# Optimization experiments

Measured on AMD Instinct MI355X. Metric: run time of the kernel, lower is better.

## Reference

```python
import jax, jax.numpy as jnp
import numpy as np

B, S, H = 8, 2048, 1024
W_SCALE = 0.02  # small init keeps the 2048-step recurrence numerically stable


def setup_inputs() -> dict:
    key = jax.random.key(0)
    ks = jax.random.split(key, 6)
    x = jax.random.normal(ks[0], (B, S, H), dtype=jnp.float32)
    h0 = jnp.zeros((B, H), dtype=jnp.float32)
    # torch Linear y = x @ W.T + b; we store pre-transposed [in, out] matrices
    W_in = jax.random.normal(ks[1], (H, 3 * H), dtype=jnp.float32) * W_SCALE
    b_in = jnp.zeros((3 * H,), dtype=jnp.float32)
    W_gate = jax.random.normal(ks[2], (H, 2 * H), dtype=jnp.float32) * W_SCALE
    b_gate = jnp.zeros((2 * H,), dtype=jnp.float32)
    W_rec = jax.random.normal(ks[3], (H, H), dtype=jnp.float32) * W_SCALE
    b_rec = jnp.zeros((H,), dtype=jnp.float32)
    W_out = jax.random.normal(ks[4], (H, H), dtype=jnp.float32) * W_SCALE
    b_out = jnp.zeros((H,), dtype=jnp.float32)
    return {"x": x, "h0": h0, "W_in": W_in, "b_in": b_in,
            "W_gate": W_gate, "b_gate": b_gate, "W_rec": W_rec, "b_rec": b_rec,
            "W_out": W_out, "b_out": b_out}


def reference(x, h0, W_in, b_in, W_gate, b_gate, W_rec, b_rec, W_out, b_out):
    # input projection, chunk into u, v, w and activate (swish)
    feats = x @ W_in + b_in                      # [B,S,3H]
    u, v, w = jnp.split(feats, 3, axis=-1)
    drive = jax.nn.silu(u) * jax.nn.silu(v) + w  # (1-gate) branch, [B,S,H]

    def step(h, d_t):
        g = h @ W_gate + b_gate                  # [B,2H]
        gv, gt = jnp.split(g, 2, axis=-1)
        gate = jax.nn.sigmoid(gv) * jax.nn.silu(gt)  # GLU gate
        new_h = gate * (h @ W_rec + b_rec) + (1.0 - gate) * d_t
        # dropout is identity in eval mode
        return new_h, new_h

    final_h, hs = jax.lax.scan(step, h0, jnp.swapaxes(drive, 0, 1))  # hs: [S,B,H]
    hs = jnp.swapaxes(hs, 0, 1)                  # [B,S,H]
    out = hs @ W_out + b_out                     # per-timestep output_proj, batched
    return out, final_h
```

## Files before the change

### kernel.cpp

```cpp
#include <hip/hip_runtime.h>

typedef short short8 __attribute__((ext_vector_type(8)));
typedef __bf16 bf16x8 __attribute__((ext_vector_type(8)));
typedef float f32x4 __attribute__((ext_vector_type(4)));
typedef float f32x4v __attribute__((ext_vector_type(4)));
typedef unsigned short u16x4 __attribute__((ext_vector_type(4)));
typedef unsigned int uint2v __attribute__((ext_vector_type(2)));
typedef unsigned long long u64;

__device__ __forceinline__ unsigned short f2b(float f) {
  unsigned x = __builtin_bit_cast(unsigned, f);
  x = x + 0x7fffu + ((x >> 16) & 1u);
  return (unsigned short)(x >> 16);
}
__device__ __forceinline__ float b2f(unsigned short u) {
  unsigned x = ((unsigned)u) << 16;
  return __builtin_bit_cast(float, x);
}
__device__ __forceinline__ f32x4 mfma16(short8 a, short8 b, f32x4 c) {
  return __builtin_amdgcn_mfma_f32_16x16x32_bf16(
      __builtin_bit_cast(bf16x8, a), __builtin_bit_cast(bf16x8, b), c, 0, 0, 0);
}
typedef const __attribute__((address_space(1))) void* gas_p;
typedef __attribute__((address_space(3))) void* las_p;
__device__ __forceinline__ void gload_lds16(const void* g, void* l) {
  __builtin_amdgcn_global_load_lds((gas_p)g, (las_p)l, 16, 0, 0);
}

__global__ __launch_bounds__(256) void k_cvt_bf16(const float* __restrict__ in,
                                                  unsigned short* __restrict__ out,
                                                  int n4) {
  int i = blockIdx.x * 256 + threadIdx.x;
  if (i >= n4) return;
  f32x4v v = *(const f32x4v*)(in + (size_t)i * 4);
  u16x4 o;
  o[0] = f2b(v[0]); o[1] = f2b(v[1]); o[2] = f2b(v[2]); o[3] = f2b(v[3]);
  *(u16x4*)(out + (size_t)i * 4) = o;
}

__global__ __launch_bounds__(256) void k_init_hq(const float* __restrict__ h0,
                                                 unsigned int* __restrict__ hq) {
  int idx = blockIdx.x * 256 + threadIdx.x;
  if (idx >= 8192) return;
  int b = idx >> 10, i = idx & 1023;
  hq[(size_t)b * 2048 + i] = (unsigned int)f2b(h0[idx]);
  hq[(size_t)b * 2048 + 1024 + i] = 0u;
}

__global__ __launch_bounds__(256) void k_transpose_bf16(const float* __restrict__ in,
                                                        unsigned short* __restrict__ out,
                                                        int R, int C) {
  __shared__ unsigned short tile[32][33];
  int c0 = blockIdx.x * 32, r0 = blockIdx.y * 32;
  int tx = threadIdx.x & 31, ty = threadIdx.x >> 5;
#pragma unroll
  for (int i = 0; i < 4; i++) {
    int r = ty + i * 8;
    tile[r][tx] = f2b(in[(size_t)(r0 + r) * C + c0 + tx]);
  }
  __syncthreads();
#pragma unroll
  for (int i = 0; i < 4; i++) {
    int rr = ty + i * 8;
    out[(size_t)(c0 + rr) * R + r0 + tx] = tile[tx][rr];
  }
}

__global__ __launch_bounds__(256) void k_gemm_drive(const unsigned short* __restrict__ xb,
                                                    const unsigned short* __restrict__ WinT,
                                                    const float* __restrict__ b_in,
                                                    unsigned short* __restrict__ drive) {
  __shared__ unsigned short At[128 * 32];
  __shared__ unsigned short Bt[3][64 * 32];
  const int tid = threadIdx.x;
  const int w = tid >> 6, l = tid & 63;
  const int wm = w >> 1, wn = w & 1;
  const int lr = l & 15, lk = (l >> 4) * 8;
  const int m0 = blockIdx.x * 128;
  const int j0 = blockIdx.y * 64;
  f32x4 acc[3][4][2];
#pragma unroll
  for (int s = 0; s < 3; s++)
#pragma unroll
    for (int mi = 0; mi < 4; mi++)
#pragma unroll
      for (int ni = 0; ni < 2; ni++)
#pragma unroll
        for (int e = 0; e < 4; e++) acc[s][mi][ni][e] = 0.f;

  const int sr = tid >> 2;
  const int skb = (tid & 3) * 8;
  for (int kt = 0; kt < 32; kt++) {
    const int k0 = kt * 32;
    gload_lds16(xb + (size_t)(m0 + sr) * 1024 + k0 + skb, &At[w * 512]);
    gload_lds16(xb + (size_t)(m0 + 64 + sr) * 1024 + k0 + skb, &At[2048 + w * 512]);
#pragma unroll
    for (int s = 0; s < 3; s++)
      gload_lds16(WinT + (size_t)(s * 1024 + j0 + sr) * 1024 + k0 + skb, &Bt[s][w * 512]);
    __syncthreads();
    short8 Af[4], Bf[3][2];
#pragma unroll
    for (int mi = 0; mi < 4; mi++)
      Af[mi] = *(const short8*)&At[(wm * 64 + mi * 16 + lr) * 32 + lk];
#pragma unroll
    for (int s = 0; s < 3; s++)
#pragma unroll
      for (int ni = 0; ni < 2; ni++)
        Bf[s][ni] = *(const short8*)&Bt[s][(wn * 32 + ni * 16 + lr) * 32 + lk];
#pragma unroll
    for (int s = 0; s < 3; s++)
#pragma unroll
      for (int mi = 0; mi < 4; mi++)
#pragma unroll
        for (int ni = 0; ni < 2; ni++)
          acc[s][mi][ni] = mfma16(Af[mi], Bf[s][ni], acc[s][mi][ni]);
    __syncthreads();
  }
#pragma unroll
  for (int ni = 0; ni < 2; ni++) {
    const int c = j0 + wn * 32 + ni * 16 + lr;
    const float bu = b_in[c], bv = b_in[1024 + c], bw = b_in[2048 + c];
#pragma unroll
    for (int mi = 0; mi < 4; mi++) {
      const int r0 = m0 + wm * 64 + mi * 16 + (l >> 4) * 4;
#pragma unroll
      for (int e = 0; e < 4; e++) {
        float u = acc[0][mi][ni][e] + bu;
        float v = acc[1][mi][ni][e] + bv;
        float wv = acc[2][mi][ni][e] + bw;
        float su = u / (1.f + __expf(-u));
        float sv = v / (1.f + __expf(-v));
        drive[(size_t)(r0 + e) * 1024 + c] = f2b(su * sv + wv);
      }
    }
  }
}

__global__ __launch_bounds__(1024, 4) void k_scan(const unsigned short* __restrict__ WgT,
                                                  const unsigned short* __restrict__ WrT,
                                                  const float* __restrict__ b_gate,
                                                  const float* __restrict__ b_rec,
                                                  const unsigned short* __restrict__ drive,
                                                  unsigned int* __restrict__ hq,
                                                  unsigned short* __restrict__ hs,
                                                  float* __restrict__ final_h) {
  const int g = blockIdx.x;
  const int r = g >> 5;
  const int s = g & 31;
  const int tid = threadIdx.x;
  const int w = tid >> 6, l = tid & 63;

  __shared__ unsigned int tileh[2][512];
  __shared__ float buf[2][4][3][32];

  const int mat = w >> 2, kq = w & 3;
  const int lr = l & 15, ko = l >> 4;
  const bool av = (lr == 0);
  short8 Breg[2][8];
  if (w < 12) {
    const unsigned short* WT = (mat == 2) ? WrT : WgT;
    const int rowbase = ((mat == 1) ? 1024 : 0) + s * 32;
#pragma unroll
    for (int tile = 0; tile < 2; ++tile)
#pragma unroll
      for (int ks = 0; ks < 8; ++ks)
        Breg[tile][ks] = *(const short8*)&WT[(size_t)(rowbase + tile * 16 + lr) * 1024 +
                                             kq * 256 + ks * 32 + ko * 8];
  }

  const bool isld = tid >= 768;
  const int q = tid - 768;

  const bool isfin = tid < 32;
  const int fcol = s * 32 + tid;
  float bgv = 0.f, bgt = 0.f, brc = 0.f;
  if (isfin) { bgv = b_gate[fcol]; bgt = b_gate[1024 + fcol]; brc = b_rec[fcol]; }

  for (int t = 0; t < 2048; ++t) {
    const int p = t & 1;
    unsigned short dpf[2] = {0, 0};
    if (isfin) {
      dpf[0] = drive[(size_t)((2 * r) * 2048 + t) * 1024 + fcol];
      dpf[1] = drive[(size_t)((2 * r + 1) * 2048 + t) * 1024 + fcol];
    }

#pragma unroll
    for (int ab = 0; ab < 2; ++ab) {
      const int b = 2 * r + ab;

      if (isld) {
        const unsigned tg = (unsigned)t;
        const u64* hb = (const u64*)(hq + (size_t)(b * 2 + p) * 1024);
        u64 v0 = 0, v1 = 0;
        unsigned pend = 3u;
        do {
          if (pend & 1u)
            v0 = __hip_atomic_load(hb + 2 * q, __ATOMIC_RELAXED,
                                   __HIP_MEMORY_SCOPE_AGENT);
          if (pend & 2u)
            v1 = __hip_atomic_load(hb + 2 * q + 1, __ATOMIC_RELAXED,
                                   __HIP_MEMORY_SCOPE_AGENT);
          unsigned np = 0;
          if ((((unsigned)v0 >> 16) != tg) | (((unsigned)(v0 >> 32) >> 16) != tg))
            np |= 1u;
          if ((((unsigned)v1 >> 16) != tg) | (((unsigned)(v1 >> 32) >> 16) != tg))
            np |= 2u;
          pend = np;
        } while (pend);
        uint2v pk;
        pk[0] = __builtin_amdgcn_perm((unsigned)(v0 >> 32), (unsigned)v0, 0x05040100u);
        pk[1] = __builtin_amdgcn_perm((unsigned)(v1 >> 32), (unsigned)v1, 0x05040100u);
        *(uint2v*)&tileh[ab][2 * q] = pk;
      }
      __syncthreads();

      if (w < 12) {
        f32x4 a0, a1;
#pragma unroll
        for (int e = 0; e < 4; ++e) { a0[e] = 0.f; a1[e] = 0.f; }
        const char* base = (const char*)&tileh[ab][0] + kq * 512 + ko * 16;
#pragma unroll
        for (int ks = 0; ks < 8; ++ks) {
          short8 Af;
#pragma unroll
          for (int e = 0; e < 8; ++e) Af[e] = 0;
          if (av) Af = *(const short8*)(base + ks * 64);
          a0 = mfma16(Af, Breg[0][ks], a0);
          a1 = mfma16(Af, Breg[1][ks], a1);
        }
        if (l < 16) {
          buf[ab][kq][mat][l] = a0[0];
          buf[ab][kq][mat][16 + l] = a1[0];
        }
      }
      __syncthreads();

      if (isfin) {
        const float gv = ((buf[ab][0][0][tid] + buf[ab][1][0][tid]) +
                          (buf[ab][2][0][tid] + buf[ab][3][0][tid])) + bgv;
        const float gt = ((buf[ab][0][1][tid] + buf[ab][1][1][tid]) +
                          (buf[ab][2][1][tid] + buf[ab][3][1][tid])) + bgt;
        const float rc = ((buf[ab][0][2][tid] + buf[ab][1][2][tid]) +
                          (buf[ab][2][2][tid] + buf[ab][3][2][tid])) + brc;
        const float sgv = 1.f / (1.f + __expf(-gv));
        const float sgt = 1.f / (1.f + __expf(-gt));
        const float gate = sgv * gt * sgt;
        const float nh = gate * rc + (1.f - gate) * b2f(dpf[ab]);
        const unsigned short nhb = f2b(nh);
        __hip_atomic_store(hq + (size_t)(b * 2 + (p ^ 1)) * 1024 + fcol,
                           (((unsigned)(t + 1)) << 16) | (unsigned)nhb,
                           __ATOMIC_RELAXED, __HIP_MEMORY_SCOPE_AGENT);
        hs[(size_t)(b * 2048 + t) * 1024 + fcol] = nhb;
        if (t == 2047) final_h[b * 1024 + fcol] = nh;
      }
    }
  }
}

__global__ __launch_bounds__(256) void k_gemm_out(const unsigned short* __restrict__ hs,
                                                  const unsigned short* __restrict__ WoT,
                                                  const float* __restrict__ b_out,
                                                  float* __restrict__ out) {
  __shared__ unsigned short At[128 * 32];
  __shared__ unsigned short Bt[128 * 32];
  const int tid = threadIdx.x;
  const int w = tid >> 6, l = tid & 63;
  const int wm = w >> 1, wn = w & 1;
  const int lr = l & 15, lk = (l >> 4) * 8;
  const int m0 = blockIdx.x * 128;
  const int n0 = blockIdx.y * 128;
  f32x4 acc[4][4];
#pragma unroll
  for (int mi = 0; mi < 4; mi++)
#pragma unroll
    for (int ni = 0; ni < 4; ni++)
#pragma unroll
      for (int e = 0; e < 4; e++) acc[mi][ni][e] = 0.f;

  const int sr = tid >> 2;
  const int skb = (tid & 3) * 8;
  for (int kt = 0; kt < 32; kt++) {
    const int k0 = kt * 32;
    gload_lds16(hs + (size_t)(m0 + sr) * 1024 + k0 + skb, &At[w * 512]);
    gload_lds16(hs + (size_t)(m0 + 64 + sr) * 1024 + k0 + skb, &At[2048 + w * 512]);
    gload_lds16(WoT + (size_t)(n0 + sr) * 1024 + k0 + skb, &Bt[w * 512]);
    gload_lds16(WoT + (size_t)(n0 + 64 + sr) * 1024 + k0 + skb, &Bt[2048 + w * 512]);
    __syncthreads();
    short8 Af[4], Bf[4];
#pragma unroll
    for (int mi = 0; mi < 4; mi++)
      Af[mi] = *(const short8*)&At[(wm * 64 + mi * 16 + lr) * 32 + lk];
#pragma unroll
    for (int ni = 0; ni < 4; ni++)
      Bf[ni] = *(const short8*)&Bt[(wn * 64 + ni * 16 + lr) * 32 + lk];
#pragma unroll
    for (int mi = 0; mi < 4; mi++)
#pragma unroll
      for (int ni = 0; ni < 4; ni++)
        acc[mi][ni] = mfma16(Af[mi], Bf[ni], acc[mi][ni]);
    __syncthreads();
  }
#pragma unroll
  for (int ni = 0; ni < 4; ni++) {
    const int c = n0 + wn * 64 + ni * 16 + lr;
    const float bo = b_out[c];
#pragma unroll
    for (int mi = 0; mi < 4; mi++) {
      const int r0 = m0 + wm * 64 + mi * 16 + (l >> 4) * 4;
#pragma unroll
      for (int e = 0; e < 4; e++)
        out[(size_t)(r0 + e) * 1024 + c] = acc[mi][ni][e] + bo;
    }
  }
}

extern "C" void kernel_launch(void* const* d_in, const int* in_sizes, int n_in,
                              void* d_out, int out_size, void* d_ws, size_t ws_size,
                              hipStream_t stream) {
  const float* x      = (const float*)d_in[0];
  const float* h0     = (const float*)d_in[1];
  const float* W_in   = (const float*)d_in[2];
  const float* b_in   = (const float*)d_in[3];
  const float* W_gate = (const float*)d_in[4];
  const float* b_gate = (const float*)d_in[5];
  const float* W_rec  = (const float*)d_in[6];
  const float* b_rec  = (const float*)d_in[7];
  const float* W_out  = (const float*)d_in[8];
  const float* b_out  = (const float*)d_in[9];
  float* outp = (float*)d_out;

  size_t off = 0;
  auto alloc = [&](size_t bytes) {
    void* p = (char*)d_ws + off;
    off += (bytes + 255) & ~(size_t)255;
    return p;
  };
  unsigned short* xb    = (unsigned short*)alloc((size_t)16777216 * 2);
  unsigned short* WinT  = (unsigned short*)alloc((size_t)3072 * 1024 * 2);
  unsigned short* WgT   = (unsigned short*)alloc((size_t)2048 * 1024 * 2);
  unsigned short* WrT   = (unsigned short*)alloc((size_t)1024 * 1024 * 2);
  unsigned short* WoT   = (unsigned short*)alloc((size_t)1024 * 1024 * 2);
  unsigned short* drive = (unsigned short*)alloc((size_t)16777216 * 2);
  unsigned short* hs    = (unsigned short*)alloc((size_t)16777216 * 2);
  unsigned int*   hq    = (unsigned int*)alloc((size_t)8 * 2 * 1024 * 4);

  k_cvt_bf16<<<16384, 256, 0, stream>>>(x, xb, 4194304);
  k_transpose_bf16<<<dim3(96, 32), 256, 0, stream>>>(W_in, WinT, 1024, 3072);
  k_transpose_bf16<<<dim3(64, 32), 256, 0, stream>>>(W_gate, WgT, 1024, 2048);
  k_transpose_bf16<<<dim3(32, 32), 256, 0, stream>>>(W_rec, WrT, 1024, 1024);
  k_transpose_bf16<<<dim3(32, 32), 256, 0, stream>>>(W_out, WoT, 1024, 1024);
  k_init_hq<<<32, 256, 0, stream>>>(h0, hq);

  k_gemm_drive<<<dim3(128, 16), 256, 0, stream>>>(xb, WinT, b_in, drive);
  k_scan<<<128, 1024, 0, stream>>>(WgT, WrT, b_gate, b_rec, drive, hq,
                                   hs, outp + 16777216);
  k_gemm_out<<<dim3(128, 8), 256, 0, stream>>>(hs, WoT, b_out, outp);
}
```

Measured before the change: 5.029 ms.

## Interleave two batch rows in scan to overlap polling with MFMA

Restructures the persistent recurrence kernel to 512 threads with 6 MFMA waves, each holding a half-K slice of weights, and 2 polling waves that each fetch 4 packed h values. Polling for one batch row's next hidden state is now placed in the same phase as the finish of the other row, so cross-block latency is hidden behind the other row's work. Drive values are also staged into shared memory by the idle polling waves. This trades more registers per wave and a different sync pattern for less serialized wait per timestep.

```diff
diff --git a/kernel.cpp b/kernel.cpp
--- a/kernel.cpp
+++ b/kernel.cpp
@@ -5,7 +5,7 @@
 typedef float f32x4 __attribute__((ext_vector_type(4)));
 typedef float f32x4v __attribute__((ext_vector_type(4)));
 typedef unsigned short u16x4 __attribute__((ext_vector_type(4)));
-typedef unsigned int uint2v __attribute__((ext_vector_type(2)));
+typedef unsigned int u32x4 __attribute__((ext_vector_type(4)));
 typedef unsigned long long u64;
 
 __device__ __forceinline__ unsigned short f2b(float f) {
@@ -136,124 +136,141 @@
   }
 }
 
-__global__ __launch_bounds__(1024, 4) void k_scan(const unsigned short* __restrict__ WgT,
-                                                  const unsigned short* __restrict__ WrT,
-                                                  const float* __restrict__ b_gate,
-                                                  const float* __restrict__ b_rec,
-                                                  const unsigned short* __restrict__ drive,
-                                                  unsigned int* __restrict__ hq,
-                                                  unsigned short* __restrict__ hs,
-                                                  float* __restrict__ final_h) {
+__global__ __launch_bounds__(512, 1) void k_scan(const unsigned short* __restrict__ WgT,
+                                                 const unsigned short* __restrict__ WrT,
+                                                 const float* __restrict__ b_gate,
+                                                 const float* __restrict__ b_rec,
+                                                 const unsigned short* __restrict__ drive,
+                                                 unsigned int* __restrict__ hq,
+                                                 unsigned short* __restrict__ hs,
+                                                 float* __restrict__ final_h) {
   const int g = blockIdx.x;
   const int r = g >> 5;
   const int s = g & 31;
   const int tid = threadIdx.x;
   const int w = tid >> 6, l = tid & 63;
+  const int bA = 2 * r, bB = 2 * r + 1;
 
   __shared__ unsigned int tileh[2][512];
-  __shared__ float buf[2][4][3][32];
-
-  const int mat = w >> 2, kq = w & 3;
+  __shared__ float buf[2][2][3][32];
+  __shared__ unsigned short dd[2][32];
+
+  const int mat = w >> 1, kh = w & 1;
   const int lr = l & 15, ko = l >> 4;
   const bool av = (lr == 0);
-  short8 Breg[2][8];
-  if (w < 12) {
+  short8 Breg0[16], Breg1[16];
+  if (w < 6) {
     const unsigned short* WT = (mat == 2) ? WrT : WgT;
     const int rowbase = ((mat == 1) ? 1024 : 0) + s * 32;
 #pragma unroll
-    for (int tile = 0; tile < 2; ++tile)
-#pragma unroll
-      for (int ks = 0; ks < 8; ++ks)
-        Breg[tile][ks] = *(const short8*)&WT[(size_t)(rowbase + tile * 16 + lr) * 1024 +
-                                             kq * 256 + ks * 32 + ko * 8];
-  }
-
-  const bool isld = tid >= 768;
-  const int q = tid - 768;
-
-  const bool isfin = tid < 32;
-  const int fcol = s * 32 + tid;
+    for (int ks = 0; ks < 16; ++ks) {
+      Breg0[ks] = *(const short8*)&WT[(size_t)(rowbase + lr) * 1024 +
+                                      kh * 512 + ks * 32 + ko * 8];
+      Breg1[ks] = *(const short8*)&WT[(size_t)(rowbase + 16 + lr) * 1024 +
+                                      kh * 512 + ks * 32 + ko * 8];
+    }
+  }
+
+  const bool ispl = (w >= 6);
+  const int P = ((w - 6) << 6) | l;
+
+  const bool isfin = (w == 0) && (l < 32);
+  const int fcol = s * 32 + l;
   float bgv = 0.f, bgt = 0.f, brc = 0.f;
   if (isfin) { bgv = b_gate[fcol]; bgt = b_gate[1024 + fcol]; brc = b_rec[fcol]; }
 
+  auto poll4 = [&](const u64* base, unsigned tg, unsigned int* dst) {
+    const u64* p = base + 4 * P;
+    u64 v[4];
+    unsigned pend = 0xFu;
+    do {
+      unsigned np = 0;
+#pragma unroll
+      for (int j = 0; j < 4; ++j)
+        if ((pend >> j) & 1)
+          v[j] = __hip_atomic_load(p + j, __ATOMIC_RELAXED,
+                                   __HIP_MEMORY_SCOPE_AGENT);
+#pragma unroll
+      for (int j = 0; j < 4; ++j)
+        if ((pend >> j) & 1) {
+          if ((((unsigned)v[j] >> 16) != tg) |
+              (((unsigned)(v[j] >> 32) >> 16) != tg))
+            np |= 1u << j;
+        }
+      pend = np;
+    } while (pend);
+    u32x4 pk;
+#pragma unroll
+    for (int j = 0; j < 4; ++j)
+      pk[j] = __builtin_amdgcn_perm((unsigned)(v[j] >> 32), (unsigned)v[j],
+                                    0x05040100u);
+    *(u32x4*)&dst[4 * P] = pk;
+  };
+
+  auto mfma_phase = [&](int X) {
+    f32x4 a0, a1, c0, c1;
+#pragma unroll
+    for (int e = 0; e < 4; ++e) { a0[e] = 0.f; a1[e] = 0.f; c0[e] = 0.f; c1[e] = 0.f; }
+    const char* base = (const char*)&tileh[X][0] + kh * 1024 + ko * 16;
+#pragma unroll
+    for (int ks = 0; ks < 16; ++ks) {
+      short8 Af;
+#pragma unroll
+      for (int e = 0; e < 8; ++e) Af[e] = 0;
+      if (av) Af = *(const short8*)(base + ks * 64);
+      if (ks & 1) { a1 = mfma16(Af, Breg0[ks], a1); c1 = mfma16(Af, Breg1[ks], c1); }
+      else        { a0 = mfma16(Af, Breg0[ks], a0); c0 = mfma16(Af, Breg1[ks], c0); }
+    }
+    if (l < 16) {
+      buf[X][kh][mat][l] = a0[0] + a1[0];
+      buf[X][kh][mat][16 + l] = c0[0] + c1[0];
+    }
+  };
+
+  auto finish = [&](int X, int b, int t) {
+    const float gv = buf[X][0][0][l] + buf[X][1][0][l] + bgv;
+    const float gt = buf[X][0][1][l] + buf[X][1][1][l] + bgt;
+    const float rc = buf[X][0][2][l] + buf[X][1][2][l] + brc;
+    const float sgv = 1.f / (1.f + __expf(-gv));
+    const float sgt = 1.f / (1.f + __expf(-gt));
+    const float gate = sgv * gt * sgt;
+    const float nh = gate * rc + (1.f - gate) * b2f(dd[X][l]);
+    const unsigned short nhb = f2b(nh);
+    __hip_atomic_store(hq + (size_t)(b * 2 + ((t + 1) & 1)) * 1024 + fcol,
+                       (((unsigned)(t + 1)) << 16) | (unsigned)nhb,
+                       __ATOMIC_RELAXED, __HIP_MEMORY_SCOPE_AGENT);
+    hs[(size_t)(b * 2048 + t) * 1024 + fcol] = nhb;
+    if (t == 2047) final_h[b * 1024 + fcol] = nh;
+  };
+
+  if (ispl) {
+    poll4((const u64*)(hq + (size_t)(bA * 2) * 1024), 0u, &tileh[0][0]);
+    poll4((const u64*)(hq + (size_t)(bB * 2) * 1024), 0u, &tileh[1][0]);
+  }
+  __syncthreads();
+
   for (int t = 0; t < 2048; ++t) {
-    const int p = t & 1;
-    unsigned short dpf[2] = {0, 0};
-    if (isfin) {
-      dpf[0] = drive[(size_t)((2 * r) * 2048 + t) * 1024 + fcol];
-      dpf[1] = drive[(size_t)((2 * r + 1) * 2048 + t) * 1024 + fcol];
-    }
-
-#pragma unroll
-    for (int ab = 0; ab < 2; ++ab) {
-      const int b = 2 * r + ab;
-
-      if (isld) {
-        const unsigned tg = (unsigned)t;
-        const u64* hb = (const u64*)(hq + (size_t)(b * 2 + p) * 1024);
-        u64 v0 = 0, v1 = 0;
-        unsigned pend = 3u;
-        do {
-          if (pend & 1u)
-            v0 = __hip_atomic_load(hb + 2 * q, __ATOMIC_RELAXED,
-                                   __HIP_MEMORY_SCOPE_AGENT);
-          if (pend & 2u)
-            v1 = __hip_atomic_load(hb + 2 * q + 1, __ATOMIC_RELAXED,
-                                   __HIP_MEMORY_SCOPE_AGENT);
-          unsigned np = 0;
-          if ((((unsigned)v0 >> 16) != tg) | (((unsigned)(v0 >> 32) >> 16) != tg))
-            np |= 1u;
-          if ((((unsigned)v1 >> 16) != tg) | (((unsigned)(v1 >> 32) >> 16) != tg))
-            np |= 2u;
-          pend = np;
-        } while (pend);
-        uint2v pk;
-        pk[0] = __builtin_amdgcn_perm((unsigned)(v0 >> 32), (unsigned)v0, 0x05040100u);
-        pk[1] = __builtin_amdgcn_perm((unsigned)(v1 >> 32), (unsigned)v1, 0x05040100u);
-        *(uint2v*)&tileh[ab][2 * q] = pk;
-      }
-      __syncthreads();
-
-      if (w < 12) {
-        f32x4 a0, a1;
-#pragma unroll
-        for (int e = 0; e < 4; ++e) { a0[e] = 0.f; a1[e] = 0.f; }
-        const char* base = (const char*)&tileh[ab][0] + kq * 512 + ko * 16;
-#pragma unroll
-        for (int ks = 0; ks < 8; ++ks) {
-          short8 Af;
-#pragma unroll
-          for (int e = 0; e < 8; ++e) Af[e] = 0;
-          if (av) Af = *(const short8*)(base + ks * 64);
-          a0 = mfma16(Af, Breg[0][ks], a0);
-          a1 = mfma16(Af, Breg[1][ks], a1);
-        }
-        if (l < 16) {
-          buf[ab][kq][mat][l] = a0[0];
-          buf[ab][kq][mat][16 + l] = a1[0];
-        }
-      }
-      __syncthreads();
-
-      if (isfin) {
-        const float gv = ((buf[ab][0][0][tid] + buf[ab][1][0][tid]) +
-                          (buf[ab][2][0][tid] + buf[ab][3][0][tid])) + bgv;
-        const float gt = ((buf[ab][0][1][tid] + buf[ab][1][1][tid]) +
-                          (buf[ab][2][1][tid] + buf[ab][3][1][tid])) + bgt;
-        const float rc = ((buf[ab][0][2][tid] + buf[ab][1][2][tid]) +
-                          (buf[ab][2][2][tid] + buf[ab][3][2][tid])) + brc;
-        const float sgv = 1.f / (1.f + __expf(-gv));
-        const float sgt = 1.f / (1.f + __expf(-gt));
-        const float gate = sgv * gt * sgt;
-        const float nh = gate * rc + (1.f - gate) * b2f(dpf[ab]);
-        const unsigned short nhb = f2b(nh);
-        __hip_atomic_store(hq + (size_t)(b * 2 + (p ^ 1)) * 1024 + fcol,
-                           (((unsigned)(t + 1)) << 16) | (unsigned)nhb,
-                           __ATOMIC_RELAXED, __HIP_MEMORY_SCOPE_AGENT);
-        hs[(size_t)(b * 2048 + t) * 1024 + fcol] = nhb;
-        if (t == 2047) final_h[b * 1024 + fcol] = nh;
-      }
-    }
+    if (w < 6) mfma_phase(0);
+    else if (l < 32) {
+      if (w == 6) dd[0][l] = drive[((size_t)bA * 2048 + t) * 1024 + s * 32 + l];
+      else        dd[1][l] = drive[((size_t)bB * 2048 + t) * 1024 + s * 32 + l];
+    }
+    __syncthreads();
+
+    if (isfin) finish(0, bA, t);
+    if (ispl && t > 0)
+      poll4((const u64*)(hq + (size_t)(bB * 2 + (t & 1)) * 1024), (unsigned)t,
+            &tileh[1][0]);
+    __syncthreads();
+
+    if (w < 6) mfma_phase(1);
+    __syncthreads();
+
+    if (isfin) finish(1, bB, t);
+    if (ispl && t < 2047)
+      poll4((const u64*)(hq + (size_t)(bA * 2 + ((t + 1) & 1)) * 1024),
+            (unsigned)(t + 1), &tileh[0][0]);
+    __syncthreads();
   }
 }
 
@@ -352,7 +369,7 @@
   k_init_hq<<<32, 256, 0, stream>>>(h0, hq);
 
   k_gemm_drive<<<dim3(128, 16), 256, 0, stream>>>(xb, WinT, b_in, drive);
-  k_scan<<<128, 1024, 0, stream>>>(WgT, WrT, b_gate, b_rec, drive, hq,
-                                   hs, outp + 16777216);
+  k_scan<<<128, 512, 0, stream>>>(WgT, WrT, b_gate, b_rec, drive, hq,
+                                  hs, outp + 16777216);
   k_gemm_out<<<dim3(128, 8), 256, 0, stream>>>(hs, WoT, b_out, outp);
 }
```

Measured after the change: 6.613 ms. 1.32x slower.
